# Kernel tuning notes

Hardware: AMD Instinct MI355X
Metric: run time of the kernel (lower is better)

Reference implementation:

```python
import jax, jax.numpy as jnp
import numpy as np

MODEL_SIZE = 1024
N_HEAD = 16
D_K = MODEL_SIZE // N_HEAD
B, S = 2, 2048


def setup_inputs() -> dict:
    key = jax.random.key(0)
    ks = jax.random.split(key, 10)
    scale = 1.0 / np.sqrt(MODEL_SIZE)
    q = jax.random.normal(ks[0], (B, S, MODEL_SIZE), dtype=jnp.float32)
    k = jax.random.normal(ks[1], (B, S, MODEL_SIZE), dtype=jnp.float32)
    v = jax.random.normal(ks[2], (B, S, MODEL_SIZE), dtype=jnp.float32)
    mask = jax.random.bernoulli(ks[3], 0.1, (B, S, S))
    Wq = jax.random.normal(ks[4], (MODEL_SIZE, MODEL_SIZE), dtype=jnp.float32) * scale
    bq = jnp.zeros((MODEL_SIZE,), dtype=jnp.float32)
    Wout = jax.random.normal(ks[5], (MODEL_SIZE, MODEL_SIZE), dtype=jnp.float32) * scale
    bout = jnp.zeros((MODEL_SIZE,), dtype=jnp.float32)
    gamma = jnp.ones((MODEL_SIZE,), dtype=jnp.float32)
    beta = jnp.zeros((MODEL_SIZE,), dtype=jnp.float32)
    return {"q": q, "k": k, "v": v, "mask": mask, "Wq": Wq, "bq": bq,
            "Wout": Wout, "bout": bout, "gamma": gamma, "beta": beta}


def _split_heads(x, seq_len):
    # [B, S, D] -> [B, S, h, d_k] -> [B, h, S, d_k] -> [B*h, S, d_k]
    b = x.shape[0]
    return x.reshape(b, seq_len, N_HEAD, D_K).transpose(0, 2, 1, 3).reshape(b * N_HEAD, seq_len, D_K)


def reference(q, k, v, mask, Wq, bq, Wout, bout, gamma, beta):
    residual = q
    len_q, len_k = q.shape[1], k.shape[1]
    # NOTE: faithful to source — linear_q projects q, k AND v.
    qp = _split_heads(q @ Wq.T + bq, len_q)
    kp = _split_heads(k @ Wq.T + bq, len_k)
    vp = _split_heads(v @ Wq.T + bq, len_k)
    # scores: [B*h, len_q, len_k], scale = sqrt(model_size) per source quirk
    attn = jnp.einsum('bqd,bkd->bqk', qp, kp) / jnp.sqrt(jnp.float32(MODEL_SIZE))
    # mask.repeat(h,1,1): tiles head-major -> [h*B, len_q, len_k]
    mask_t = jnp.tile(mask, (N_HEAD, 1, 1))
    attn = jnp.where(mask_t, jnp.float32(-1e18), attn)
    w = jax.nn.softmax(attn, axis=-1)
    out = jnp.einsum('bqk,bkd->bqd', w, vp)  # [B*h, len_q, d_k]
    b = residual.shape[0]
    out = out.reshape(b, N_HEAD, len_q, D_K).transpose(0, 2, 1, 3).reshape(b, len_q, MODEL_SIZE)
    out = out @ Wout.T + bout
    x = residual + out
    mu = jnp.mean(x, axis=-1, keepdims=True)
    var = jnp.var(x, axis=-1, keepdims=True)
    out = (x - mu) / jnp.sqrt(var + 1e-6) * gamma + beta
    return (out, w)
```

## Files before the change

### kernel.cpp

```cpp
#include <hip/hip_runtime.h>
#include <hip/hip_bf16.h>

#define SEQ 2048
#define DIM 1024
#define NH 16
#define DK 64
#define NBH 32
#define MROWS 4096

typedef __attribute__((ext_vector_type(8))) short bf16x8_t;
typedef __attribute__((ext_vector_type(4))) float f32x4_t;

__device__ __forceinline__ unsigned short f2bf(float f) {
  union { float f; unsigned u; } v; v.f = f;
  unsigned r = v.u + 0x7FFFu + ((v.u >> 16) & 1u);
  return (unsigned short)(r >> 16);
}

struct Cvt5 {
  const float* src[5];
  unsigned short* dst[5];
  int n4[5];
};

__global__ __launch_bounds__(256) void cvt5_kernel(Cvt5 P) {
  int i = blockIdx.x * 256 + threadIdx.x;
  int off = 0;
#pragma unroll
  for (int s = 0; s < 5; ++s) {
    int n4 = P.n4[s];
    int j = i - off;
    if (j >= 0 && j < n4) {
      float4 v = reinterpret_cast<const float4*>(P.src[s])[j];
      ushort4 o = make_ushort4(f2bf(v.x), f2bf(v.y), f2bf(v.z), f2bf(v.w));
      reinterpret_cast<ushort4*>(P.dst[s])[j] = o;
    }
    off += n4;
  }
}

__global__ void detect_mask_kernel(const unsigned char* m, int* flag) {
  int v = 0;
  for (int i = threadIdx.x; i < 8192; i += 64)
    if ((i & 3) && m[i]) v = 1;
  unsigned long long b = __ballot(v);
  if (threadIdx.x == 0) *flag = (b != 0ull) ? 1 : 0;
}

__global__ __launch_bounds__(256) void cvt_mask_kernel(const void* msrc, unsigned char* mdst, const int* flag) {
  int i = blockIdx.x * 256 + threadIdx.x;
  if (*flag) {
    reinterpret_cast<uchar4*>(mdst)[i] = reinterpret_cast<const uchar4*>(msrc)[i];
  } else {
    int4 v = reinterpret_cast<const int4*>(msrc)[i];
    reinterpret_cast<uchar4*>(mdst)[i] =
        make_uchar4((unsigned char)(v.x != 0), (unsigned char)(v.y != 0),
                    (unsigned char)(v.z != 0), (unsigned char)(v.w != 0));
  }
}

struct Proj3 {
  const unsigned short* A[3];
  unsigned short* dst[3];
};

__global__ __launch_bounds__(256) void proj_gemm_kernel(Proj3 P, const unsigned short* W, const float* bias) {
  const int mtile = blockIdx.x, ntile = blockIdx.y, which = blockIdx.z;
  const unsigned short* A = P.A[which];
  unsigned short* dst = P.dst[which];
  const int wv = threadIdx.x >> 6;
  const int l = threadIdx.x & 63;
  const int lr = l & 15, lg = l >> 4;
  const int n0 = ntile * 64;
  const unsigned short* Ap  = A + (size_t)(mtile * 64 + wv * 16 + lr) * DIM + lg * 8;
  const unsigned short* Wp0 = W + (size_t)(n0 +  0 + lr) * DIM + lg * 8;
  const unsigned short* Wp1 = W + (size_t)(n0 + 16 + lr) * DIM + lg * 8;
  const unsigned short* Wp2 = W + (size_t)(n0 + 32 + lr) * DIM + lg * 8;
  const unsigned short* Wp3 = W + (size_t)(n0 + 48 + lr) * DIM + lg * 8;
  f32x4_t a0 = {0.f, 0.f, 0.f, 0.f}, a1 = a0, a2 = a0, a3 = a0;
  for (int k0 = 0; k0 < DIM; k0 += 32) {
    bf16x8_t a = *reinterpret_cast<const bf16x8_t*>(Ap + k0);
    a0 = __builtin_amdgcn_mfma_f32_16x16x32_bf16(a, *reinterpret_cast<const bf16x8_t*>(Wp0 + k0), a0, 0, 0, 0);
    a1 = __builtin_amdgcn_mfma_f32_16x16x32_bf16(a, *reinterpret_cast<const bf16x8_t*>(Wp1 + k0), a1, 0, 0, 0);
    a2 = __builtin_amdgcn_mfma_f32_16x16x32_bf16(a, *reinterpret_cast<const bf16x8_t*>(Wp2 + k0), a2, 0, 0, 0);
    a3 = __builtin_amdgcn_mfma_f32_16x16x32_bf16(a, *reinterpret_cast<const bf16x8_t*>(Wp3 + k0), a3, 0, 0, 0);
  }
  const int mbase = mtile * 64 + wv * 16 + lg * 4;
  const float b0 = bias[n0 +  0 + lr];
  const float b1 = bias[n0 + 16 + lr];
  const float b2 = bias[n0 + 32 + lr];
  const float b3 = bias[n0 + 48 + lr];
#pragma unroll
  for (int r = 0; r < 4; ++r) {
    const int m = mbase + r;
    const int b = m >> 11, s = m & (SEQ - 1);
    unsigned short* drow = dst + ((size_t)(b * NH + ntile) * SEQ + s) * DK;
    drow[ 0 + lr] = f2bf(a0[r] + b0);
    drow[16 + lr] = f2bf(a1[r] + b1);
    drow[32 + lr] = f2bf(a2[r] + b2);
    drow[48 + lr] = f2bf(a3[r] + b3);
  }
}

__global__ __launch_bounds__(256) void transpose_v_kernel(const unsigned short* vp, unsigned short* vpT) {
  const int stile = blockIdx.x, bh = blockIdx.y;
  const int s0 = stile * 64;
  __shared__ unsigned short ld[64][66];
  const int t = threadIdx.x;
  const int r = t >> 2, c0 = (t & 3) * 16;
  const unsigned short* src = vp + ((size_t)bh * SEQ + s0 + r) * DK + c0;
  bf16x8_t v0 = *reinterpret_cast<const bf16x8_t*>(src);
  bf16x8_t v1 = *reinterpret_cast<const bf16x8_t*>(src + 8);
#pragma unroll
  for (int j = 0; j < 8; ++j) {
    ld[r][c0 + j] = (unsigned short)v0[j];
    ld[r][c0 + 8 + j] = (unsigned short)v1[j];
  }
  __syncthreads();
  bf16x8_t w0, w1;
#pragma unroll
  for (int j = 0; j < 8; ++j) {
    w0[j] = (short)ld[c0 + j][r];
    w1[j] = (short)ld[c0 + 8 + j][r];
  }
  unsigned short* dstp = vpT + ((size_t)bh * DK + r) * SEQ + s0 + c0;
  *reinterpret_cast<bf16x8_t*>(dstp) = w0;
  *reinterpret_cast<bf16x8_t*>(dstp + 8) = w1;
}

__global__ __launch_bounds__(256) void attn_kernel(const unsigned short* qp, const unsigned short* kp,
                                                   const unsigned short* vpT, const unsigned char* maskb,
                                                   float* wout, unsigned short* attn_o) {
  const int qtile = blockIdx.x, bh = blockIdx.y;
  const int wv = threadIdx.x >> 6;
  const int l = threadIdx.x & 63;
  const int lr = l & 15, lg = l >> 4;
  const int qrow0 = qtile * 64 + wv * 16;
  const unsigned short* qptr = qp + ((size_t)bh * SEQ + qrow0 + lr) * DK + lg * 8;
  const bf16x8_t aq0 = *reinterpret_cast<const bf16x8_t*>(qptr);
  const bf16x8_t aq1 = *reinterpret_cast<const bf16x8_t*>(qptr + 32);
  const int crow0 = qrow0 + lg * 4;
  const int mb = bh & 1;
  const unsigned char* mr0 = maskb + ((size_t)mb * SEQ + crow0) * SEQ;
  const unsigned char* mr1 = mr0 + SEQ;
  const unsigned char* mr2 = mr0 + 2 * SEQ;
  const unsigned char* mr3 = mr0 + 3 * SEQ;
  const unsigned short* kbase = kp + (size_t)bh * SEQ * DK + lg * 8;
  const float scale = 0.03125f;

  float s0 = 0.f, s1 = 0.f, s2 = 0.f, s3 = 0.f;
  for (int c0 = 0; c0 < SEQ; c0 += 16) {
    const unsigned short* kpp = kbase + (size_t)(c0 + lr) * DK;
    f32x4_t acc = {0.f, 0.f, 0.f, 0.f};
    acc = __builtin_amdgcn_mfma_f32_16x16x32_bf16(aq0, *reinterpret_cast<const bf16x8_t*>(kpp), acc, 0, 0, 0);
    acc = __builtin_amdgcn_mfma_f32_16x16x32_bf16(aq1, *reinterpret_cast<const bf16x8_t*>(kpp + 32), acc, 0, 0, 0);
    const int kc = c0 + lr;
    s0 += mr0[kc] ? 0.f : __expf(acc[0] * scale);
    s1 += mr1[kc] ? 0.f : __expf(acc[1] * scale);
    s2 += mr2[kc] ? 0.f : __expf(acc[2] * scale);
    s3 += mr3[kc] ? 0.f : __expf(acc[3] * scale);
  }
#pragma unroll
  for (int sh = 1; sh < 16; sh <<= 1) {
    s0 += __shfl_xor(s0, sh);
    s1 += __shfl_xor(s1, sh);
    s2 += __shfl_xor(s2, sh);
    s3 += __shfl_xor(s3, sh);
  }
  const float i0 = 1.f / s0, i1 = 1.f / s1, i2 = 1.f / s2, i3 = 1.f / s3;

  float* wr0 = wout + ((size_t)bh * SEQ + crow0) * SEQ;
  float* wr1 = wr0 + SEQ;
  float* wr2 = wr0 + 2 * SEQ;
  float* wr3 = wr0 + 3 * SEQ;
  const unsigned short* vbase = vpT + (size_t)bh * DK * SEQ + lg * 8;
  __shared__ __align__(16) unsigned short Plds[4][16][32];
  f32x4_t o0 = {0.f, 0.f, 0.f, 0.f}, o1 = o0, o2 = o0, o3 = o0;
  for (int k0 = 0; k0 < SEQ; k0 += 32) {
#pragma unroll
    for (int half = 0; half < 2; ++half) {
      const int c0 = k0 + half * 16;
      const unsigned short* kpp = kbase + (size_t)(c0 + lr) * DK;
      f32x4_t acc = {0.f, 0.f, 0.f, 0.f};
      acc = __builtin_amdgcn_mfma_f32_16x16x32_bf16(aq0, *reinterpret_cast<const bf16x8_t*>(kpp), acc, 0, 0, 0);
      acc = __builtin_amdgcn_mfma_f32_16x16x32_bf16(aq1, *reinterpret_cast<const bf16x8_t*>(kpp + 32), acc, 0, 0, 0);
      const int kc = c0 + lr;
      const float p0 = mr0[kc] ? 0.f : __expf(acc[0] * scale) * i0;
      const float p1 = mr1[kc] ? 0.f : __expf(acc[1] * scale) * i1;
      const float p2 = mr2[kc] ? 0.f : __expf(acc[2] * scale) * i2;
      const float p3 = mr3[kc] ? 0.f : __expf(acc[3] * scale) * i3;
      wr0[kc] = p0;
      wr1[kc] = p1;
      wr2[kc] = p2;
      wr3[kc] = p3;
      Plds[wv][lg * 4 + 0][half * 16 + lr] = f2bf(p0);
      Plds[wv][lg * 4 + 1][half * 16 + lr] = f2bf(p1);
      Plds[wv][lg * 4 + 2][half * 16 + lr] = f2bf(p2);
      Plds[wv][lg * 4 + 3][half * 16 + lr] = f2bf(p3);
    }
    __syncthreads();
    const bf16x8_t pa = *reinterpret_cast<const bf16x8_t*>(&Plds[wv][lr][lg * 8]);
    o0 = __builtin_amdgcn_mfma_f32_16x16x32_bf16(pa, *reinterpret_cast<const bf16x8_t*>(vbase + (size_t)( 0 + lr) * SEQ + k0), o0, 0, 0, 0);
    o1 = __builtin_amdgcn_mfma_f32_16x16x32_bf16(pa, *reinterpret_cast<const bf16x8_t*>(vbase + (size_t)(16 + lr) * SEQ + k0), o1, 0, 0, 0);
    o2 = __builtin_amdgcn_mfma_f32_16x16x32_bf16(pa, *reinterpret_cast<const bf16x8_t*>(vbase + (size_t)(32 + lr) * SEQ + k0), o2, 0, 0, 0);
    o3 = __builtin_amdgcn_mfma_f32_16x16x32_bf16(pa, *reinterpret_cast<const bf16x8_t*>(vbase + (size_t)(48 + lr) * SEQ + k0), o3, 0, 0, 0);
    __syncthreads();
  }
  const int b = bh >> 4, h = bh & 15;
  unsigned short* obase = attn_o + ((size_t)b * SEQ + crow0) * DIM + h * DK;
#pragma unroll
  for (int r = 0; r < 4; ++r) {
    unsigned short* orow = obase + (size_t)r * DIM;
    orow[ 0 + lr] = f2bf(o0[r]);
    orow[16 + lr] = f2bf(o1[r]);
    orow[32 + lr] = f2bf(o2[r]);
    orow[48 + lr] = f2bf(o3[r]);
  }
}

__global__ __launch_bounds__(256) void out_gemm_kernel(const unsigned short* A, const unsigned short* W,
                                                       const float* bias, const float* resid, float* X) {
  const int mtile = blockIdx.x, ntile = blockIdx.y;
  const int wv = threadIdx.x >> 6;
  const int l = threadIdx.x & 63;
  const int lr = l & 15, lg = l >> 4;
  const int n0 = ntile * 64;
  const unsigned short* Ap  = A + (size_t)(mtile * 64 + wv * 16 + lr) * DIM + lg * 8;
  const unsigned short* Wp0 = W + (size_t)(n0 +  0 + lr) * DIM + lg * 8;
  const unsigned short* Wp1 = W + (size_t)(n0 + 16 + lr) * DIM + lg * 8;
  const unsigned short* Wp2 = W + (size_t)(n0 + 32 + lr) * DIM + lg * 8;
  const unsigned short* Wp3 = W + (size_t)(n0 + 48 + lr) * DIM + lg * 8;
  f32x4_t a0 = {0.f, 0.f, 0.f, 0.f}, a1 = a0, a2 = a0, a3 = a0;
  for (int k0 = 0; k0 < DIM; k0 += 32) {
    bf16x8_t a = *reinterpret_cast<const bf16x8_t*>(Ap + k0);
    a0 = __builtin_amdgcn_mfma_f32_16x16x32_bf16(a, *reinterpret_cast<const bf16x8_t*>(Wp0 + k0), a0, 0, 0, 0);
    a1 = __builtin_amdgcn_mfma_f32_16x16x32_bf16(a, *reinterpret_cast<const bf16x8_t*>(Wp1 + k0), a1, 0, 0, 0);
    a2 = __builtin_amdgcn_mfma_f32_16x16x32_bf16(a, *reinterpret_cast<const bf16x8_t*>(Wp2 + k0), a2, 0, 0, 0);
    a3 = __builtin_amdgcn_mfma_f32_16x16x32_bf16(a, *reinterpret_cast<const bf16x8_t*>(Wp3 + k0), a3, 0, 0, 0);
  }
  const int mbase = mtile * 64 + wv * 16 + lg * 4;
  const float b0 = bias[n0 +  0 + lr];
  const float b1 = bias[n0 + 16 + lr];
  const float b2 = bias[n0 + 32 + lr];
  const float b3 = bias[n0 + 48 + lr];
#pragma unroll
  for (int r = 0; r < 4; ++r) {
    const int m = mbase + r;
    float* xrow = X + (size_t)m * DIM;
    const float* rrow = resid + (size_t)m * DIM;
    xrow[n0 +  0 + lr] = a0[r] + b0 + rrow[n0 +  0 + lr];
    xrow[n0 + 16 + lr] = a1[r] + b1 + rrow[n0 + 16 + lr];
    xrow[n0 + 32 + lr] = a2[r] + b2 + rrow[n0 + 32 + lr];
    xrow[n0 + 48 + lr] = a3[r] + b3 + rrow[n0 + 48 + lr];
  }
}

__global__ __launch_bounds__(256) void ln_kernel(const float* X, const float* gamma, const float* beta, float* out) {
  const int row = blockIdx.x;
  const int t = threadIdx.x;
  float4 v = reinterpret_cast<const float4*>(X + (size_t)row * DIM)[t];
  float s1 = v.x + v.y + v.z + v.w;
  float s2 = v.x * v.x + v.y * v.y + v.z * v.z + v.w * v.w;
#pragma unroll
  for (int sh = 1; sh < 64; sh <<= 1) {
    s1 += __shfl_xor(s1, sh);
    s2 += __shfl_xor(s2, sh);
  }
  __shared__ float p1[4], p2[4];
  if ((t & 63) == 0) { p1[t >> 6] = s1; p2[t >> 6] = s2; }
  __syncthreads();
  s1 = p1[0] + p1[1] + p1[2] + p1[3];
  s2 = p2[0] + p2[1] + p2[2] + p2[3];
  const float mu = s1 * (1.f / DIM);
  const float var = s2 * (1.f / DIM) - mu * mu;
  const float rstd = rsqrtf(var + 1e-6f);
  float4 g = reinterpret_cast<const float4*>(gamma)[t];
  float4 be = reinterpret_cast<const float4*>(beta)[t];
  float4 o;
  o.x = (v.x - mu) * rstd * g.x + be.x;
  o.y = (v.y - mu) * rstd * g.y + be.y;
  o.z = (v.z - mu) * rstd * g.z + be.z;
  o.w = (v.w - mu) * rstd * g.w + be.w;
  reinterpret_cast<float4*>(out + (size_t)row * DIM)[t] = o;
}

extern "C" void kernel_launch(void* const* d_in, const int* in_sizes, int n_in,
                              void* d_out, int out_size, void* d_ws, size_t ws_size,
                              hipStream_t stream) {
  const float* q     = (const float*)d_in[0];
  const float* k     = (const float*)d_in[1];
  const float* v     = (const float*)d_in[2];
  const void*  mask  = d_in[3];
  const float* Wq    = (const float*)d_in[4];
  const float* bq    = (const float*)d_in[5];
  const float* Wout  = (const float*)d_in[6];
  const float* bout  = (const float*)d_in[7];
  const float* gamma = (const float*)d_in[8];
  const float* beta  = (const float*)d_in[9];

  float* out0 = (float*)d_out;
  float* wout = out0 + (size_t)2 * SEQ * DIM;

  char* ws = (char*)d_ws;
  size_t off = 0;
  auto alloc = [&](size_t bytes) -> char* {
    char* p = ws + off;
    off += (bytes + 255) & ~(size_t)255;
    return p;
  };
  int* flag            = (int*)alloc(256);
  unsigned short* qb   = (unsigned short*)alloc((size_t)MROWS * DIM * 2);
  unsigned short* kb   = (unsigned short*)alloc((size_t)MROWS * DIM * 2);
  unsigned short* vb   = (unsigned short*)alloc((size_t)MROWS * DIM * 2);
  unsigned short* Wqb  = (unsigned short*)alloc((size_t)DIM * DIM * 2);
  unsigned short* Wob  = (unsigned short*)alloc((size_t)DIM * DIM * 2);
  unsigned short* qp   = (unsigned short*)alloc((size_t)NBH * SEQ * DK * 2);
  unsigned short* kp   = (unsigned short*)alloc((size_t)NBH * SEQ * DK * 2);
  unsigned short* vp   = (unsigned short*)alloc((size_t)NBH * SEQ * DK * 2);
  unsigned short* vpT  = (unsigned short*)alloc((size_t)NBH * SEQ * DK * 2);
  unsigned short* ao   = (unsigned short*)alloc((size_t)MROWS * DIM * 2);
  unsigned char* maskb = (unsigned char*)alloc((size_t)2 * SEQ * SEQ);
  float* X             = (float*)alloc((size_t)MROWS * DIM * 4);

  Cvt5 C;
  C.src[0] = q;    C.dst[0] = qb;  C.n4[0] = MROWS * DIM / 4;
  C.src[1] = k;    C.dst[1] = kb;  C.n4[1] = MROWS * DIM / 4;
  C.src[2] = v;    C.dst[2] = vb;  C.n4[2] = MROWS * DIM / 4;
  C.src[3] = Wq;   C.dst[3] = Wqb; C.n4[3] = DIM * DIM / 4;
  C.src[4] = Wout; C.dst[4] = Wob; C.n4[4] = DIM * DIM / 4;
  const int totalN4 = 3 * (MROWS * DIM / 4) + 2 * (DIM * DIM / 4);
  cvt5_kernel<<<(totalN4 + 255) / 256, 256, 0, stream>>>(C);

  detect_mask_kernel<<<1, 64, 0, stream>>>((const unsigned char*)mask, flag);
  cvt_mask_kernel<<<(2 * SEQ * SEQ / 4 + 255) / 256, 256, 0, stream>>>(mask, maskb, flag);

  Proj3 P;
  P.A[0] = qb; P.dst[0] = qp;
  P.A[1] = kb; P.dst[1] = kp;
  P.A[2] = vb; P.dst[2] = vp;
  proj_gemm_kernel<<<dim3(MROWS / 64, DIM / 64, 3), 256, 0, stream>>>(P, Wqb, bq);

  transpose_v_kernel<<<dim3(SEQ / 64, NBH), 256, 0, stream>>>(vp, vpT);

  attn_kernel<<<dim3(SEQ / 64, NBH), 256, 0, stream>>>(qp, kp, vpT, maskb, wout, ao);

  out_gemm_kernel<<<dim3(MROWS / 64, DIM / 64), 256, 0, stream>>>(ao, Wob, bout, q, X);

  ln_kernel<<<MROWS, 256, 0, stream>>>(X, gamma, beta, out0);
}
```

Baseline: 1.328 ms.

## Tile projection and output GEMMs 128x128 via LDS with direct global-to-LDS loads

Both the projection and output GEMMs now share a 128x128 block-tiled core. It stages A and W tiles in LDS using global_load_lds, and each wave computes a 4x4 grid of MFMA tiles, which increases operand reuse over the previous register-only 64x64 tiles. The attention kernel drops its two per-step __syncthreads, relying on the fact that each wave only touches its own P slice. Mask detection now reads 32-bit words instead of bytes. The single-buffered LDS loop still synchronises on every K step, and the strided epilogue stores stay uncoalesced.

```diff
diff --git a/kernel.cpp b/kernel.cpp
--- a/kernel.cpp
+++ b/kernel.cpp
@@ -7,6 +7,9 @@
 #define DK 64
 #define NBH 32
 #define MROWS 4096
+#define BM 128
+#define BN 128
+#define BK 32
 
 typedef __attribute__((ext_vector_type(8))) short bf16x8_t;
 typedef __attribute__((ext_vector_type(4))) float f32x4_t;
@@ -15,6 +18,11 @@
   union { float f; unsigned u; } v; v.f = f;
   unsigned r = v.u + 0x7FFFu + ((v.u >> 16) & 1u);
   return (unsigned short)(r >> 16);
+}
+
+__device__ __forceinline__ void gload16(const unsigned short* g, unsigned short* l) {
+  __builtin_amdgcn_global_load_lds((const __attribute__((address_space(1))) void*)g,
+                                   (__attribute__((address_space(3))) void*)l, 16, 0, 0);
 }
 
 struct Cvt5 {
@@ -39,11 +47,11 @@
   }
 }
 
-__global__ void detect_mask_kernel(const unsigned char* m, int* flag) {
-  int v = 0;
-  for (int i = threadIdx.x; i < 8192; i += 64)
-    if ((i & 3) && m[i]) v = 1;
-  unsigned long long b = __ballot(v);
+__global__ void detect_mask_kernel(const unsigned int* m, int* flag) {
+  unsigned acc = 0;
+  for (int i = threadIdx.x; i < 2048; i += 64)
+    acc |= (m[i] & 0xFFFFFF00u);
+  unsigned long long b = __ballot(acc != 0);
   if (threadIdx.x == 0) *flag = (b != 0ull) ? 1 : 0;
 }
 
@@ -59,6 +67,35 @@
   }
 }
 
+__device__ __forceinline__ void gemm_core_128(const unsigned short* A, const unsigned short* Wb,
+                                              unsigned short* AL, unsigned short* BL,
+                                              f32x4_t acc[4][4], int wv, int lane,
+                                              int wr, int wc, int lr, int lg) {
+  for (int k0 = 0; k0 < DIM; k0 += BK) {
+    if (k0) __syncthreads();
+#pragma unroll
+    for (int j = 0; j < 2; ++j) {
+      const int e = wv * 1024 + j * 512 + lane * 8;
+      const int row = e >> 5, kk = e & 31;
+      gload16(A + (size_t)row * DIM + k0 + kk, AL + wv * 1024 + j * 512);
+      gload16(Wb + (size_t)row * DIM + k0 + kk, BL + wv * 1024 + j * 512);
+    }
+    __syncthreads();
+    bf16x8_t a[4], b[4];
+#pragma unroll
+    for (int m = 0; m < 4; ++m)
+      a[m] = *reinterpret_cast<const bf16x8_t*>(AL + (wr * 64 + m * 16 + lr) * BK + lg * 8);
+#pragma unroll
+    for (int n = 0; n < 4; ++n)
+      b[n] = *reinterpret_cast<const bf16x8_t*>(BL + (wc * 64 + n * 16 + lr) * BK + lg * 8);
+#pragma unroll
+    for (int m = 0; m < 4; ++m)
+#pragma unroll
+      for (int n = 0; n < 4; ++n)
+        acc[m][n] = __builtin_amdgcn_mfma_f32_16x16x32_bf16(a[m], b[n], acc[m][n], 0, 0, 0);
+  }
+}
+
 struct Proj3 {
   const unsigned short* A[3];
   unsigned short* dst[3];
@@ -66,39 +103,61 @@
 
 __global__ __launch_bounds__(256) void proj_gemm_kernel(Proj3 P, const unsigned short* W, const float* bias) {
   const int mtile = blockIdx.x, ntile = blockIdx.y, which = blockIdx.z;
-  const unsigned short* A = P.A[which];
+  const unsigned short* A = P.A[which] + (size_t)(mtile * BM) * DIM;
+  const unsigned short* Wb = W + (size_t)(ntile * BN) * DIM;
+  __shared__ __align__(16) unsigned short AL[BM * BK];
+  __shared__ __align__(16) unsigned short BL[BN * BK];
+  const int tid = threadIdx.x;
+  const int wv = tid >> 6, lane = tid & 63;
+  const int lr = lane & 15, lg = lane >> 4;
+  const int wr = wv >> 1, wc = wv & 1;
+  f32x4_t acc[4][4] = {};
+  gemm_core_128(A, Wb, AL, BL, acc, wv, lane, wr, wc, lr, lg);
+
   unsigned short* dst = P.dst[which];
-  const int wv = threadIdx.x >> 6;
-  const int l = threadIdx.x & 63;
-  const int lr = l & 15, lg = l >> 4;
-  const int n0 = ntile * 64;
-  const unsigned short* Ap  = A + (size_t)(mtile * 64 + wv * 16 + lr) * DIM + lg * 8;
-  const unsigned short* Wp0 = W + (size_t)(n0 +  0 + lr) * DIM + lg * 8;
-  const unsigned short* Wp1 = W + (size_t)(n0 + 16 + lr) * DIM + lg * 8;
-  const unsigned short* Wp2 = W + (size_t)(n0 + 32 + lr) * DIM + lg * 8;
-  const unsigned short* Wp3 = W + (size_t)(n0 + 48 + lr) * DIM + lg * 8;
-  f32x4_t a0 = {0.f, 0.f, 0.f, 0.f}, a1 = a0, a2 = a0, a3 = a0;
-  for (int k0 = 0; k0 < DIM; k0 += 32) {
-    bf16x8_t a = *reinterpret_cast<const bf16x8_t*>(Ap + k0);
-    a0 = __builtin_amdgcn_mfma_f32_16x16x32_bf16(a, *reinterpret_cast<const bf16x8_t*>(Wp0 + k0), a0, 0, 0, 0);
-    a1 = __builtin_amdgcn_mfma_f32_16x16x32_bf16(a, *reinterpret_cast<const bf16x8_t*>(Wp1 + k0), a1, 0, 0, 0);
-    a2 = __builtin_amdgcn_mfma_f32_16x16x32_bf16(a, *reinterpret_cast<const bf16x8_t*>(Wp2 + k0), a2, 0, 0, 0);
-    a3 = __builtin_amdgcn_mfma_f32_16x16x32_bf16(a, *reinterpret_cast<const bf16x8_t*>(Wp3 + k0), a3, 0, 0, 0);
-  }
-  const int mbase = mtile * 64 + wv * 16 + lg * 4;
-  const float b0 = bias[n0 +  0 + lr];
-  const float b1 = bias[n0 + 16 + lr];
-  const float b2 = bias[n0 + 32 + lr];
-  const float b3 = bias[n0 + 48 + lr];
-#pragma unroll
-  for (int r = 0; r < 4; ++r) {
-    const int m = mbase + r;
-    const int b = m >> 11, s = m & (SEQ - 1);
-    unsigned short* drow = dst + ((size_t)(b * NH + ntile) * SEQ + s) * DK;
-    drow[ 0 + lr] = f2bf(a0[r] + b0);
-    drow[16 + lr] = f2bf(a1[r] + b1);
-    drow[32 + lr] = f2bf(a2[r] + b2);
-    drow[48 + lr] = f2bf(a3[r] + b3);
+#pragma unroll
+  for (int n = 0; n < 4; ++n) {
+    const int dfull = ntile * BN + wc * 64 + n * 16 + lr;
+    const int h = dfull >> 6, d = dfull & 63;
+    const float bv = bias[dfull];
+#pragma unroll
+    for (int m = 0; m < 4; ++m) {
+#pragma unroll
+      for (int r = 0; r < 4; ++r) {
+        const int mg = mtile * BM + wr * 64 + m * 16 + lg * 4 + r;
+        const int b_ = mg >> 11, s = mg & (SEQ - 1);
+        dst[((size_t)(b_ * NH + h) * SEQ + s) * DK + d] = f2bf(acc[m][n][r] + bv);
+      }
+    }
+  }
+}
+
+__global__ __launch_bounds__(256) void out_gemm_kernel(const unsigned short* Ain, const unsigned short* W,
+                                                       const float* bias, const float* resid, float* X) {
+  const int mtile = blockIdx.x, ntile = blockIdx.y;
+  const unsigned short* A = Ain + (size_t)(mtile * BM) * DIM;
+  const unsigned short* Wb = W + (size_t)(ntile * BN) * DIM;
+  __shared__ __align__(16) unsigned short AL[BM * BK];
+  __shared__ __align__(16) unsigned short BL[BN * BK];
+  const int tid = threadIdx.x;
+  const int wv = tid >> 6, lane = tid & 63;
+  const int lr = lane & 15, lg = lane >> 4;
+  const int wr = wv >> 1, wc = wv & 1;
+  f32x4_t acc[4][4] = {};
+  gemm_core_128(A, Wb, AL, BL, acc, wv, lane, wr, wc, lr, lg);
+
+#pragma unroll
+  for (int n = 0; n < 4; ++n) {
+    const int c = ntile * BN + wc * 64 + n * 16 + lr;
+    const float bv = bias[c];
+#pragma unroll
+    for (int m = 0; m < 4; ++m) {
+#pragma unroll
+      for (int r = 0; r < 4; ++r) {
+        const int mg = mtile * BM + wr * 64 + m * 16 + lg * 4 + r;
+        X[(size_t)mg * DIM + c] = acc[m][n][r] + bv + resid[(size_t)mg * DIM + c];
+      }
+    }
   }
 }
 
@@ -198,13 +257,11 @@
       Plds[wv][lg * 4 + 2][half * 16 + lr] = f2bf(p2);
       Plds[wv][lg * 4 + 3][half * 16 + lr] = f2bf(p3);
     }
-    __syncthreads();
     const bf16x8_t pa = *reinterpret_cast<const bf16x8_t*>(&Plds[wv][lr][lg * 8]);
     o0 = __builtin_amdgcn_mfma_f32_16x16x32_bf16(pa, *reinterpret_cast<const bf16x8_t*>(vbase + (size_t)( 0 + lr) * SEQ + k0), o0, 0, 0, 0);
     o1 = __builtin_amdgcn_mfma_f32_16x16x32_bf16(pa, *reinterpret_cast<const bf16x8_t*>(vbase + (size_t)(16 + lr) * SEQ + k0), o1, 0, 0, 0);
     o2 = __builtin_amdgcn_mfma_f32_16x16x32_bf16(pa, *reinterpret_cast<const bf16x8_t*>(vbase + (size_t)(32 + lr) * SEQ + k0), o2, 0, 0, 0);
     o3 = __builtin_amdgcn_mfma_f32_16x16x32_bf16(pa, *reinterpret_cast<const bf16x8_t*>(vbase + (size_t)(48 + lr) * SEQ + k0), o3, 0, 0, 0);
-    __syncthreads();
   }
   const int b = bh >> 4, h = bh & 15;
   unsigned short* obase = attn_o + ((size_t)b * SEQ + crow0) * DIM + h * DK;
@@ -215,43 +272,6 @@
     orow[16 + lr] = f2bf(o1[r]);
     orow[32 + lr] = f2bf(o2[r]);
     orow[48 + lr] = f2bf(o3[r]);
-  }
-}
-
-__global__ __launch_bounds__(256) void out_gemm_kernel(const unsigned short* A, const unsigned short* W,
-                                                       const float* bias, const float* resid, float* X) {
-  const int mtile = blockIdx.x, ntile = blockIdx.y;
-  const int wv = threadIdx.x >> 6;
-  const int l = threadIdx.x & 63;
-  const int lr = l & 15, lg = l >> 4;
-  const int n0 = ntile * 64;
-  const unsigned short* Ap  = A + (size_t)(mtile * 64 + wv * 16 + lr) * DIM + lg * 8;
-  const unsigned short* Wp0 = W + (size_t)(n0 +  0 + lr) * DIM + lg * 8;
-  const unsigned short* Wp1 = W + (size_t)(n0 + 16 + lr) * DIM + lg * 8;
-  const unsigned short* Wp2 = W + (size_t)(n0 + 32 + lr) * DIM + lg * 8;
-  const unsigned short* Wp3 = W + (size_t)(n0 + 48 + lr) * DIM + lg * 8;
-  f32x4_t a0 = {0.f, 0.f, 0.f, 0.f}, a1 = a0, a2 = a0, a3 = a0;
-  for (int k0 = 0; k0 < DIM; k0 += 32) {
-    bf16x8_t a = *reinterpret_cast<const bf16x8_t*>(Ap + k0);
-    a0 = __builtin_amdgcn_mfma_f32_16x16x32_bf16(a, *reinterpret_cast<const bf16x8_t*>(Wp0 + k0), a0, 0, 0, 0);
-    a1 = __builtin_amdgcn_mfma_f32_16x16x32_bf16(a, *reinterpret_cast<const bf16x8_t*>(Wp1 + k0), a1, 0, 0, 0);
-    a2 = __builtin_amdgcn_mfma_f32_16x16x32_bf16(a, *reinterpret_cast<const bf16x8_t*>(Wp2 + k0), a2, 0, 0, 0);
-    a3 = __builtin_amdgcn_mfma_f32_16x16x32_bf16(a, *reinterpret_cast<const bf16x8_t*>(Wp3 + k0), a3, 0, 0, 0);
-  }
-  const int mbase = mtile * 64 + wv * 16 + lg * 4;
-  const float b0 = bias[n0 +  0 + lr];
-  const float b1 = bias[n0 + 16 + lr];
-  const float b2 = bias[n0 + 32 + lr];
-  const float b3 = bias[n0 + 48 + lr];
-#pragma unroll
-  for (int r = 0; r < 4; ++r) {
-    const int m = mbase + r;
-    float* xrow = X + (size_t)m * DIM;
-    const float* rrow = resid + (size_t)m * DIM;
-    xrow[n0 +  0 + lr] = a0[r] + b0 + rrow[n0 +  0 + lr];
-    xrow[n0 + 16 + lr] = a1[r] + b1 + rrow[n0 + 16 + lr];
-    xrow[n0 + 32 + lr] = a2[r] + b2 + rrow[n0 + 32 + lr];
-    xrow[n0 + 48 + lr] = a3[r] + b3 + rrow[n0 + 48 + lr];
   }
 }
 
@@ -331,20 +351,20 @@
   const int totalN4 = 3 * (MROWS * DIM / 4) + 2 * (DIM * DIM / 4);
   cvt5_kernel<<<(totalN4 + 255) / 256, 256, 0, stream>>>(C);
 
-  detect_mask_kernel<<<1, 64, 0, stream>>>((const unsigned char*)mask, flag);
+  detect_mask_kernel<<<1, 64, 0, stream>>>((const unsigned int*)mask, flag);
   cvt_mask_kernel<<<(2 * SEQ * SEQ / 4 + 255) / 256, 256, 0, stream>>>(mask, maskb, flag);
 
   Proj3 P;
   P.A[0] = qb; P.dst[0] = qp;
   P.A[1] = kb; P.dst[1] = kp;
   P.A[2] = vb; P.dst[2] = vp;
-  proj_gemm_kernel<<<dim3(MROWS / 64, DIM / 64, 3), 256, 0, stream>>>(P, Wqb, bq);
+  proj_gemm_kernel<<<dim3(MROWS / BM, DIM / BN, 3), 256, 0, stream>>>(P, Wqb, bq);
 
   transpose_v_kernel<<<dim3(SEQ / 64, NBH), 256, 0, stream>>>(vp, vpT);
 
   attn_kernel<<<dim3(SEQ / 64, NBH), 256, 0, stream>>>(qp, kp, vpT, maskb, wout, ao);
 
-  out_gemm_kernel<<<dim3(MROWS / 64, DIM / 64), 256, 0, stream>>>(ao, Wob, bout, q, X);
+  out_gemm_kernel<<<dim3(MROWS / BM, DIM / BN), 256, 0, stream>>>(ao, Wob, bout, q, X);
 
   ln_kernel<<<MROWS, 256, 0, stream>>>(X, gamma, beta, out0);
 }
```

Result: faster. 1.111 ms (-16.4%).
